# Kernel optimization log

Hardware: AMD Instinct MI355X
Metric: run time of the kernel (lower is better)

## Reference

```python
import jax, jax.numpy as jnp
import numpy as np

EPS = 1e-7
MIN_NORM = 1e-15
PROJ_EPS = 1e-5
NEG_SLOPE = 0.2
HEADS = 4


def artanh(x):
    return jnp.arctanh(jnp.clip(x, -1.0 + EPS, 1.0 - EPS))


def _norm(x):
    return jnp.clip(jnp.linalg.norm(x, axis=-1, keepdims=True), MIN_NORM)


def proj(x):
    # project onto Poincare ball (c=1)
    n = _norm(x)
    maxn = 1.0 - PROJ_EPS
    return jnp.where(n > maxn, x / n * maxn, x)


def expmap0(u):
    n = _norm(u)
    return jnp.tanh(n) * u / n


def logmap0(x):
    n = _norm(x)
    return artanh(n) * x / n


def mobius_add(x, y):
    x2 = jnp.sum(x * x, axis=-1, keepdims=True)
    y2 = jnp.sum(y * y, axis=-1, keepdims=True)
    xy = jnp.sum(x * y, axis=-1, keepdims=True)
    num = (1.0 + 2.0 * xy + y2) * x + (1.0 - x2) * y
    den = 1.0 + 2.0 * xy + x2 * y2
    return num / jnp.clip(den, MIN_NORM)


def pdist(x, y):
    # Poincare distance, c=1 -> [...,] scalar
    ma = mobius_add(-x, y)
    return 2.0 * artanh(jnp.linalg.norm(ma, axis=-1))


def mobius_scalar_mul(r, x):
    n = _norm(x)
    return jnp.tanh(r * artanh(n)) * x / n


def mobius_matvec(W, x):
    # x: [N,din], W: [dout,din]
    mx = x @ W.T
    n_x = _norm(x)
    n_mx = _norm(mx)
    return jnp.tanh(n_mx / n_x * artanh(n_x)) * mx / n_mx


def segment_softmax(logits, seg, num_segments):
    m = jax.ops.segment_max(logits, seg, num_segments=num_segments)
    m = jnp.where(jnp.isfinite(m), m, 0.0)
    e = jnp.exp(logits - m[seg])
    s = jax.ops.segment_sum(e, seg, num_segments=num_segments)
    return e / (s[seg] + 1e-16)


def setup_inputs() -> dict:
    N, E, D = 50000, 500000, 128
    H = HEADS
    Dh = D // H
    ks = jax.random.split(jax.random.key(0), 12)
    # edges without self-loops (reference re-adds them, mirroring remove/add_self_loops)
    src = jax.random.randint(ks[0], (E,), 0, N)
    off = jax.random.randint(ks[1], (E,), 1, N)
    dst = (src + off) % N
    edge_index = jnp.stack([src, dst]).astype(jnp.int32)
    x_e = 0.1 * jax.random.normal(ks[2], (N, D), dtype=jnp.float32)
    x_h = proj(expmap0(0.05 * jax.random.normal(ks[3], (N, D), dtype=jnp.float32)))
    sc = 1.0 / np.sqrt(D)
    W_e = sc * jax.random.normal(ks[4], (D, D), dtype=jnp.float32)
    b_lin_e = jnp.zeros((D,), jnp.float32)
    att_e = 0.1 * jax.random.normal(ks[5], (1, H, 2 * Dh), dtype=jnp.float32)
    b_e = jnp.zeros((D,), jnp.float32)
    W_h = sc * jax.random.normal(ks[6], (D, D), dtype=jnp.float32)
    b_lin_h = jnp.zeros((D,), jnp.float32)
    att_h = 0.1 * jax.random.normal(ks[7], (1, H, 2 * Dh), dtype=jnp.float32)
    b_h = jnp.zeros((D,), jnp.float32)
    att_hf = 0.1 * jax.random.normal(ks[8], (1, 1), dtype=jnp.float32)
    att_ef = 0.1 * jax.random.normal(ks[9], (1, 1), dtype=jnp.float32)
    return {"x_e": x_e, "x_h": x_h, "edge_index": edge_index,
            "W_e": W_e, "b_lin_e": b_lin_e, "att_e": att_e, "b_e": b_e,
            "W_h": W_h, "b_lin_h": b_lin_h, "att_h": att_h, "b_h": b_h,
            "att_hf": att_hf, "att_ef": att_ef}


def reference(x_e, x_h, edge_index, W_e, b_lin_e, att_e, b_e,
              W_h, b_lin_h, att_h, b_h, att_hf, att_ef):
    N, D = x_e.shape
    H = HEADS
    Dh = att_e.shape[-1] // 2
    loop = jnp.arange(N, dtype=edge_index.dtype)
    src = jnp.concatenate([edge_index[0], loop])  # j (source)
    dst = jnp.concatenate([edge_index[1], loop])  # i (target, softmax segment)

    # ---- Euclidean GAT branch (GATConv) ----
    xe = (x_e @ W_e.T + b_lin_e).reshape(N, H, Dh)
    a_i = jnp.sum(xe * att_e[:, :, :Dh], axis=-1)  # [N,H] target part
    a_j = jnp.sum(xe * att_e[:, :, Dh:], axis=-1)  # [N,H] source part
    alpha = jax.nn.leaky_relu(a_i[dst] + a_j[src], NEG_SLOPE)  # [E',H]
    alpha = segment_softmax(alpha, dst, N)
    agg = jax.ops.segment_sum(xe[src] * alpha[:, :, None], dst, num_segments=N)
    e_out = jax.nn.relu(agg.reshape(N, H * Dh) + b_e)

    # ---- Hyperbolic GAT branch (HGATConv with HypLinear) ----
    mv = proj(mobius_matvec(W_h, x_h))
    hb = proj(expmap0(b_lin_h))  # proj_tan0 is identity on Poincare ball
    xh = proj(mobius_add(mv, hb))  # [N,D] hyperbolic points (original_x)
    lx = logmap0(xh).reshape(N, H, Dh)
    hi = jnp.sum(lx * att_h[:, :, :Dh], axis=-1)
    hj = jnp.sum(lx * att_h[:, :, Dh:], axis=-1)
    alpha_h = hi[dst] + hj[src]  # [E',H]
    d = pdist(xh[dst], xh[src])  # [E'] hyperbolic edge distances
    d = segment_softmax(d, dst, N)[:, None]
    alpha_h = jax.nn.leaky_relu(alpha_h * d, NEG_SLOPE)
    alpha_h = segment_softmax(alpha_h, dst, N)
    agg_h = jax.ops.segment_sum(lx[src] * alpha_h[:, :, None], dst, num_segments=N)
    out_t = jax.nn.relu(agg_h.reshape(N, H * Dh) + b_h)  # tangent at origin
    h_out = proj(expmap0(out_t))

    # ---- HFusion: fuse Euclidean into hyperbolic ----
    ye = proj(expmap0(e_out))
    dist_f = (pdist(h_out, ye) * att_hf[0, 0])[:, None]  # [N,1]
    xe2 = proj(mobius_scalar_mul(dist_f, ye))
    h_fused = proj(mobius_add(h_out, xe2))

    # ---- EFusion: fuse hyperbolic into Euclidean ----
    lh = logmap0(h_out)
    de = (jnp.sum((lh - e_out) ** 2, axis=-1) * att_ef[0, 0])[:, None]
    e_fused = e_out + de * lh

    return jnp.stack([h_fused, e_fused])  # [2,N,D]
```

## Files before the change

### kernel.cpp

```cpp
#include <hip/hip_runtime.h>
#include <hip/hip_fp16.h>
#include <math.h>

typedef _Float16 h2 __attribute__((ext_vector_type(2)));
typedef _Float16 h8 __attribute__((ext_vector_type(8)));
typedef float f32x4 __attribute__((ext_vector_type(4)));

#define MAXN_BALL (1.0f - 1e-5f)
#define ART_CLIP  (1.0f - 1e-7f)
#define MAXD 48

__device__ __forceinline__ float f_rcp(float x)  { return __builtin_amdgcn_rcpf(x); }
__device__ __forceinline__ float f_exp(float x)  { return __expf(x); }
__device__ __forceinline__ float f_log(float x)  { return __logf(x); }
__device__ __forceinline__ float f_tanh(float x) {
    float ax = fabsf(x);
    float e = __expf(2.f * ax);
    float t = 1.f - 2.f * f_rcp(e + 1.f);
    return copysignf(t, x);
}
__device__ __forceinline__ float f_atanh(float x) {
    x = fminf(x, ART_CLIP);
    return 0.5f * f_log((1.f + x) * f_rcp(1.f - x));
}
__device__ __forceinline__ float leaky(float x) { return x > 0.0f ? x : 0.2f * x; }

union F4H8 { float4 f; h2 h[4]; };
union F2H4 { float2 f; h2 h[2]; };
union H8U  { h8 v; h2 h[4]; };
union H8F  { float4 f; h8 v; h2 h[4]; };

__device__ __forceinline__ h2 pk16(float x, float y) {
    union { decltype(__builtin_amdgcn_cvt_pkrtz(0.f, 0.f)) a; h2 b; } u;
    u.a = __builtin_amdgcn_cvt_pkrtz(x, y);
    return u.b;
}

__global__ __launch_bounds__(256) void k_wcvt(const float* __restrict__ W0,
                                              const float* __restrict__ W1,
                                              h2* __restrict__ W16,
                                              int* __restrict__ counts,
                                              int N, int cblocks) {
    int b = blockIdx.x, t = threadIdx.x;
    if (b < cblocks) {
        int zi = b * 256 + t;
        if (zi < N) counts[zi] = 0;
        return;
    }
    int tw = (b - cblocks) * 256 + t;
    const float* W = (tw < 2048) ? W0 : W1;
    int c = (tw & 2047) * 8;
    float4 a = *(const float4*)(W + c);
    float4 bb = *(const float4*)(W + c + 4);
    F4H8 u;
    u.h[0] = pk16(a.x, a.y);  u.h[1] = pk16(a.z, a.w);
    u.h[2] = pk16(bb.x, bb.y); u.h[3] = pk16(bb.z, bb.w);
    *(float4*)&W16[(tw >> 11) * 8192 + (c >> 1)] = u.f;
}

__global__ __launch_bounds__(256) void k_prep(const float* __restrict__ X0,
                                              const float* __restrict__ X1,
                                              const h2* __restrict__ W16,
                                              const float* __restrict__ bias0,
                                              const float* __restrict__ att_e,
                                              h2* __restrict__ Y0,
                                              h2* __restrict__ Y1,
                                              float* __restrict__ aux_j,
                                              float* __restrict__ aux_i,
                                              float* __restrict__ aux_n,
                                              const int* __restrict__ ei,
                                              int* __restrict__ counts,
                                              int* __restrict__ srcs,
                                              int N, int E) {
    int t = threadIdx.x;
    if (blockIdx.y == 2) {
        int idx = blockIdx.x * 256 + t;
        if (idx < E + N) {
            int s, d;
            if (idx < E) { s = ei[idx]; d = ei[E + idx]; } else { s = d = idx - E; }
            int p = atomicAdd(&counts[d], 1);
            if (p < MAXD) srcs[d * MAXD + p] = s;
        }
        return;
    }
    int wv = t >> 6, l = t & 63;
    int rt = blockIdx.x * 4 + wv;
    if (rt * 32 >= N) return;
    int mat = blockIdx.y;
    const float* X = mat ? X1 : X0;
    const h2* Wbase = W16 + mat * 8192;
    h2* Y = mat ? Y1 : Y0;

    int lane16 = l & 15, quad = l >> 4;
    int r0 = rt * 32 + lane16, r1 = r0 + 16;
    int rr0 = (r0 < N) ? r0 : (N - 1);
    int rr1 = (r1 < N) ? r1 : (N - 1);
    const float* Xrow0 = &X[(size_t)rr0 * 128 + quad * 8];
    const float* Xrow1 = &X[(size_t)rr1 * 128 + quad * 8];

    H8U b0r[4], b1r[4];
    float nx20 = 0.f, nx21 = 0.f;
#pragma unroll
    for (int ks = 0; ks < 4; ++ks) {
        float4 xa = *(const float4*)(Xrow0 + ks * 32);
        float4 xb = *(const float4*)(Xrow0 + ks * 32 + 4);
        if (mat) nx20 += xa.x * xa.x + xa.y * xa.y + xa.z * xa.z + xa.w * xa.w
                       + xb.x * xb.x + xb.y * xb.y + xb.z * xb.z + xb.w * xb.w;
        b0r[ks].h[0] = pk16(xa.x, xa.y); b0r[ks].h[1] = pk16(xa.z, xa.w);
        b0r[ks].h[2] = pk16(xb.x, xb.y); b0r[ks].h[3] = pk16(xb.z, xb.w);
        float4 ya = *(const float4*)(Xrow1 + ks * 32);
        float4 yb = *(const float4*)(Xrow1 + ks * 32 + 4);
        if (mat) nx21 += ya.x * ya.x + ya.y * ya.y + ya.z * ya.z + ya.w * ya.w
                       + yb.x * yb.x + yb.y * yb.y + yb.z * yb.z + yb.w * yb.w;
        b1r[ks].h[0] = pk16(ya.x, ya.y); b1r[ks].h[1] = pk16(ya.z, ya.w);
        b1r[ks].h[2] = pk16(yb.x, yb.y); b1r[ks].h[3] = pk16(yb.z, yb.w);
    }

    float pi0[4] = {0.f, 0.f, 0.f, 0.f}, pj0[4] = {0.f, 0.f, 0.f, 0.f};
    float pi1[4] = {0.f, 0.f, 0.f, 0.f}, pj1[4] = {0.f, 0.f, 0.f, 0.f};
#pragma unroll
    for (int ct = 0; ct < 8; ++ct) {
        const h2* Wrow = &Wbase[(ct * 16 + lane16) * 64 + quad * 4];
        f32x4 acc0 = {0.f, 0.f, 0.f, 0.f};
        f32x4 acc1 = {0.f, 0.f, 0.f, 0.f};
#pragma unroll
        for (int ks = 0; ks < 4; ++ks) {
            H8F a;
            a.f = *(const float4*)(Wrow + ks * 16);
            acc0 = __builtin_amdgcn_mfma_f32_16x16x32_f16(a.v, b0r[ks].v, acc0, 0, 0, 0);
            acc1 = __builtin_amdgcn_mfma_f32_16x16x32_f16(a.v, b1r[ks].v, acc1, 0, 0, 0);
        }
        int obase = ct * 16 + quad * 4;
        if (mat == 0) {
            float4 bb = *(const float4*)&bias0[obase];
            F2H4 u0, u1;
            u0.h[0] = pk16(acc0[0] + bb.x, acc0[1] + bb.y);
            u0.h[1] = pk16(acc0[2] + bb.z, acc0[3] + bb.w);
            u1.h[0] = pk16(acc1[0] + bb.x, acc1[1] + bb.y);
            u1.h[1] = pk16(acc1[2] + bb.z, acc1[3] + bb.w);
            if (r0 < N) *(float2*)&Y[(size_t)r0 * 64 + (obase >> 1)] = u0.f;
            if (r1 < N) *(float2*)&Y[(size_t)r1 * 64 + (obase >> 1)] = u1.f;
            float4 xe40 = make_float4((float)u0.h[0].x, (float)u0.h[0].y,
                                      (float)u0.h[1].x, (float)u0.h[1].y);
            float4 xe41 = make_float4((float)u1.h[0].x, (float)u1.h[0].y,
                                      (float)u1.h[1].x, (float)u1.h[1].y);
            int hd = ct >> 1, w0 = (ct & 1) * 16 + quad * 4;
            float4 aT = *(const float4*)&att_e[hd * 64 + w0];
            float4 aS = *(const float4*)&att_e[hd * 64 + 32 + w0];
            pi0[hd] += xe40.x * aT.x + xe40.y * aT.y + xe40.z * aT.z + xe40.w * aT.w;
            pj0[hd] += xe40.x * aS.x + xe40.y * aS.y + xe40.z * aS.z + xe40.w * aS.w;
            pi1[hd] += xe41.x * aT.x + xe41.y * aT.y + xe41.z * aT.z + xe41.w * aT.w;
            pj1[hd] += xe41.x * aS.x + xe41.y * aS.y + xe41.z * aS.z + xe41.w * aS.w;
        } else {
            F2H4 u0, u1;
            u0.h[0] = pk16(acc0[0], acc0[1]); u0.h[1] = pk16(acc0[2], acc0[3]);
            u1.h[0] = pk16(acc1[0], acc1[1]); u1.h[1] = pk16(acc1[2], acc1[3]);
            if (r0 < N) *(float2*)&Y[(size_t)r0 * 64 + (obase >> 1)] = u0.f;
            if (r1 < N) *(float2*)&Y[(size_t)r1 * 64 + (obase >> 1)] = u1.f;
        }
    }

    if (mat == 0) {
#pragma unroll
        for (int m = 16; m <= 32; m <<= 1) {
#pragma unroll
            for (int hd = 0; hd < 4; ++hd) {
                pi0[hd] += __shfl_xor(pi0[hd], m, 64);
                pj0[hd] += __shfl_xor(pj0[hd], m, 64);
                pi1[hd] += __shfl_xor(pi1[hd], m, 64);
                pj1[hd] += __shfl_xor(pj1[hd], m, 64);
            }
        }
        if (quad == 0) {
            if (r0 < N) {
                *(float4*)&aux_i[(size_t)r0 * 8 + 4]  = make_float4(pi0[0], pi0[1], pi0[2], pi0[3]);
                *(float4*)&aux_j[(size_t)r0 * 16 + 4] = make_float4(pj0[0], pj0[1], pj0[2], pj0[3]);
            }
            if (r1 < N) {
                *(float4*)&aux_i[(size_t)r1 * 8 + 4]  = make_float4(pi1[0], pi1[1], pi1[2], pi1[3]);
                *(float4*)&aux_j[(size_t)r1 * 16 + 4] = make_float4(pj1[0], pj1[1], pj1[2], pj1[3]);
            }
        }
    } else {
#pragma unroll
        for (int m = 16; m <= 32; m <<= 1) {
            nx20 += __shfl_xor(nx20, m, 64);
            nx21 += __shfl_xor(nx21, m, 64);
        }
        if (quad == 0) {
            if (r0 < N) aux_n[r0] = nx20;
            if (r1 < N) aux_n[r1] = nx21;
        }
    }
}

__global__ __launch_bounds__(256) void k_node1(
        const float* __restrict__ aux_n, const h2* __restrict__ mx16,
        h2* __restrict__ xh16,
        float* __restrict__ aux_j, float* __restrict__ aux_i,
        const float* __restrict__ att_h, const float* __restrict__ b_lin_h,
        int N) {
    int t = threadIdx.x;
    int sl = t & 31, ni = t >> 5;
    int i = blockIdx.x * 8 + ni;
    if (i >= N) return;
    int ht = sl >> 3, d0 = (sl & 7) * 4;

    F2H4 umx; umx.f = *(const float2*)&mx16[(size_t)i * 64 + 2 * sl];
    float4 mx4 = make_float4((float)umx.h[0].x, (float)umx.h[0].y,
                             (float)umx.h[1].x, (float)umx.h[1].y);
    float4 bv4 = *(const float4*)&b_lin_h[4 * sl];
    float nmx2 = mx4.x * mx4.x + mx4.y * mx4.y + mx4.z * mx4.z + mx4.w * mx4.w;
    float nb2  = bv4.x * bv4.x + bv4.y * bv4.y + bv4.z * bv4.z + bv4.w * bv4.w;
    float dmb  = mx4.x * bv4.x + mx4.y * bv4.y + mx4.z * bv4.z + mx4.w * bv4.w;
#pragma unroll
    for (int m = 16; m >= 1; m >>= 1) {
        nmx2 += __shfl_xor(nmx2, m, 64);
        nb2  += __shfl_xor(nb2, m, 64);
        dmb  += __shfl_xor(dmb, m, 64);
    }
    float nx2 = aux_n[i];

    float nxr = sqrtf(nx2),  nxc = fmaxf(nxr, 1e-15f);
    float nmxr = sqrtf(nmx2), nmxc = fmaxf(nmxr, 1e-15f);
    float tt = f_tanh(nmxc * f_rcp(nxc) * f_atanh(nxc));
    float c_m = tt * f_rcp(nmxc);
    float nmv = tt * (nmxr * f_rcp(nmxc));
    if (nmv > MAXN_BALL) { c_m *= MAXN_BALL / nmv; nmv = MAXN_BALL; }

    float nbr = sqrtf(nb2), nbc = fmaxf(nbr, 1e-15f);
    float tb = f_tanh(nbc);
    float c_b = tb * f_rcp(nbc);
    float nhb = tb * (nbr * f_rcp(nbc));
    if (nhb > MAXN_BALL) { c_b *= MAXN_BALL / nhb; nhb = MAXN_BALL; }

    float xy = c_m * c_b * dmb;
    float x2 = nmv * nmv, y2 = nhb * nhb;
    float den = fmaxf(1.f + 2.f * xy + x2 * y2, 1e-15f);
    float rden = f_rcp(den);
    float al = (1.f + 2.f * xy + y2) * c_m * rden;
    float be = (1.f - x2) * c_b * rden;
    float nr2 = al * al * nmx2 + 2.f * al * be * dmb + be * be * nb2;
    float nrr = sqrtf(nr2);
    if (nrr > MAXN_BALL) { float sc = MAXN_BALL / nrr; al *= sc; be *= sc; }
    float4 resv;
    resv.x = al * mx4.x + be * bv4.x; resv.y = al * mx4.y + be * bv4.y;
    resv.z = al * mx4.z + be * bv4.z; resv.w = al * mx4.w + be * bv4.w;
    F2H4 st;
    st.h[0] = pk16(resv.x, resv.y);
    st.h[1] = pk16(resv.z, resv.w);
    *(float2*)&xh16[(size_t)i * 64 + 2 * sl] = st.f;
    float4 rv = make_float4((float)st.h[0].x, (float)st.h[0].y,
                            (float)st.h[1].x, (float)st.h[1].y);

    float nr2r = rv.x * rv.x + rv.y * rv.y + rv.z * rv.z + rv.w * rv.w;
#pragma unroll
    for (int m = 16; m >= 1; m >>= 1) nr2r += __shfl_xor(nr2r, m, 64);
    float nrrr = sqrtf(nr2r);
    float nnc = fmaxf(nrrr, 1e-15f);
    float lam = f_atanh(nnc) * f_rcp(nnc);
    if (sl == 0) { aux_j[(size_t)i * 16 + 8] = lam; aux_j[(size_t)i * 16 + 9] = nr2r; }

    float4 lxv = make_float4(lam * rv.x, lam * rv.y, lam * rv.z, lam * rv.w);
    float4 ahT = *(const float4*)&att_h[ht * 64 + d0];
    float4 ahS = *(const float4*)&att_h[ht * 64 + 32 + d0];
    float qi = lxv.x * ahT.x + lxv.y * ahT.y + lxv.z * ahT.z + lxv.w * ahT.w;
    float qj = lxv.x * ahS.x + lxv.y * ahS.y + lxv.z * ahS.z + lxv.w * ahS.w;
#pragma unroll
    for (int m = 1; m <= 4; m <<= 1) { qi += __shfl_xor(qi, m, 64); qj += __shfl_xor(qj, m, 64); }
    if ((sl & 7) == 0) {
        aux_j[(size_t)i * 16 + ht] = qj;
        aux_i[(size_t)i * 8 + ht] = qi;
    }
}

__global__ __launch_bounds__(256) void k_node_final(
    const h2* __restrict__ xh16, const float* __restrict__ aux_j,
    const float* __restrict__ aux_i, const h2* __restrict__ xe16,
    const int* __restrict__ counts, const int* __restrict__ srcs,
    const float* __restrict__ b_e, const float* __restrict__ b_h,
    const float* __restrict__ att_hf, const float* __restrict__ att_ef,
    float* __restrict__ out, int N) {
    __shared__ int   s_src_all[8][MAXD];
    __shared__ float s_d_all[8][MAXD];
    __shared__ float s_ah_all[8][MAXD * 4];
    __shared__ float s_ae_all[8][MAXD * 4];

    int t = threadIdx.x;
    int sl = t & 31, ni = t >> 5;
    int i = blockIdx.x * 8 + ni;
    if (i >= N) return;
    int*   s_src = s_src_all[ni];
    float* s_d   = s_d_all[ni];
    float* s_ah  = s_ah_all[ni];
    float* s_ae  = s_ae_all[ni];

    int deg = counts[i];
    if (deg > MAXD) deg = MAXD;
    if (sl < deg)      s_src[sl]      = srcs[i * MAXD + sl];
    if (sl + 32 < deg) s_src[sl + 32] = srcs[i * MAXD + sl + 32];

    float x2i = aux_j[(uint32_t)i * 16u + 9u];
    {
        int g = sl & 7, sub = sl >> 3;
        uint32_t goff = (uint32_t)(g * 8);
        const h2* xi = &xh16[(uint32_t)i * 64u + goff];
        F4H8 us0, us1;
        us0.f = *(const float4*)xi;
        us1.f = *(const float4*)(xi + 4);
        for (int p = 0; p * 4 < deg; ++p) {
            int e = p * 4 + sub;
            bool act = e < deg;
            float dot = 0.f;
            int j = 0;
            if (act) {
                j = s_src[e];
                uint32_t oj = (uint32_t)j * 64u + goff;
                F4H8 ua, ub;
                ua.f = *(const float4*)&xh16[oj];
                ub.f = *(const float4*)&xh16[oj + 4u];
#pragma unroll
                for (int k = 0; k < 4; ++k) dot = __builtin_amdgcn_fdot2(ua.h[k], us0.h[k], dot, false);
#pragma unroll
                for (int k = 0; k < 4; ++k) dot = __builtin_amdgcn_fdot2(ub.h[k], us1.h[k], dot, false);
            }
            dot += __shfl_xor(dot, 1, 64);
            dot += __shfl_xor(dot, 2, 64);
            dot += __shfl_xor(dot, 4, 64);
            if (act && g == 0) {
                float y2 = aux_j[(uint32_t)j * 16u + 9u];
                float xy = dot;
                float A = 1.f - 2.f * xy + y2;
                float B = 1.f - x2i;
                float den = fmaxf(1.f - 2.f * xy + x2i * y2, 1e-15f);
                float num2 = fmaxf(A * A * x2i - 2.f * A * B * xy + B * B * y2, 0.f);
                float nma = fminf(sqrtf(num2) * f_rcp(den), ART_CLIP);
                s_d[e] = f_log((1.f + nma) * f_rcp(1.f - nma));
            }
        }
    }

    float eA = (sl < deg)      ? f_exp(s_d[sl])      : 0.f;
    float eB = (sl + 32 < deg) ? f_exp(s_d[sl + 32]) : 0.f;
    float ssum = eA + eB;
#pragma unroll
    for (int m = 16; m >= 1; m >>= 1) ssum += __shfl_xor(ssum, m, 64);
    float dinv = f_rcp(ssum + 1e-16f);

    float4 hi4 = *(const float4*)&aux_i[(uint32_t)i * 8u];
    float4 ai4 = *(const float4*)&aux_i[(uint32_t)i * 8u + 4u];
    float4 vh_s[2], ve_s[2];
    float lam_s[2] = {0.f, 0.f};
    float4 sh = make_float4(0.f, 0.f, 0.f, 0.f), se = sh;
#pragma unroll
    for (int s = 0; s < 2; ++s) {
        int e = sl + 32 * s;
        if (e < deg) {
            int j = s_src[e];
            float ds = (s ? eB : eA) * dinv;
            uint32_t oj = (uint32_t)j * 16u;
            float4 hj4 = *(const float4*)&aux_j[oj];
            float4 aj4 = *(const float4*)&aux_j[oj + 4u];
            lam_s[s] = aux_j[oj + 8u];
            float4 vh, ve;
            vh.x = f_exp(leaky((hi4.x + hj4.x) * ds));
            vh.y = f_exp(leaky((hi4.y + hj4.y) * ds));
            vh.z = f_exp(leaky((hi4.z + hj4.z) * ds));
            vh.w = f_exp(leaky((hi4.w + hj4.w) * ds));
            ve.x = f_exp(leaky(ai4.x + aj4.x));
            ve.y = f_exp(leaky(ai4.y + aj4.y));
            ve.z = f_exp(leaky(ai4.z + aj4.z));
            ve.w = f_exp(leaky(ai4.w + aj4.w));
            vh_s[s] = vh; ve_s[s] = ve;
            sh.x += vh.x; sh.y += vh.y; sh.z += vh.z; sh.w += vh.w;
            se.x += ve.x; se.y += ve.y; se.z += ve.z; se.w += ve.w;
        }
    }
#pragma unroll
    for (int m = 16; m >= 1; m >>= 1) {
        sh.x += __shfl_xor(sh.x, m, 64); sh.y += __shfl_xor(sh.y, m, 64);
        sh.z += __shfl_xor(sh.z, m, 64); sh.w += __shfl_xor(sh.w, m, 64);
        se.x += __shfl_xor(se.x, m, 64); se.y += __shfl_xor(se.y, m, 64);
        se.z += __shfl_xor(se.z, m, 64); se.w += __shfl_xor(se.w, m, 64);
    }
    float4 rh = make_float4(f_rcp(sh.x + 1e-16f), f_rcp(sh.y + 1e-16f),
                            f_rcp(sh.z + 1e-16f), f_rcp(sh.w + 1e-16f));
    float4 re = make_float4(f_rcp(se.x + 1e-16f), f_rcp(se.y + 1e-16f),
                            f_rcp(se.z + 1e-16f), f_rcp(se.w + 1e-16f));
#pragma unroll
    for (int s = 0; s < 2; ++s) {
        int e = sl + 32 * s;
        if (e < deg) {
            float lamj = lam_s[s];
            float4 vh = vh_s[s], ve = ve_s[s];
            vh.x *= rh.x * lamj; vh.y *= rh.y * lamj; vh.z *= rh.z * lamj; vh.w *= rh.w * lamj;
            ve.x *= re.x; ve.y *= re.y; ve.z *= re.z; ve.w *= re.w;
            *(float4*)&s_ah[e * 4] = vh;
            *(float4*)&s_ae[e * 4] = ve;
        }
    }

    int hq = sl >> 3;
    uint32_t dsl = 2u * (uint32_t)sl;
    float4 aE = make_float4(0.f, 0.f, 0.f, 0.f), aH = aE;
    int e = 0;
    for (; e + 3 < deg; e += 4) {
        int j0 = s_src[e], j1 = s_src[e + 1], j2 = s_src[e + 2], j3 = s_src[e + 3];
        uint32_t o0 = (uint32_t)j0 * 64u + dsl, o1 = (uint32_t)j1 * 64u + dsl;
        uint32_t o2 = (uint32_t)j2 * 64u + dsl, o3 = (uint32_t)j3 * 64u + dsl;
        F2H4 ux0, uh0, ux1, uh1, ux2, uh2, ux3, uh3;
        ux0.f = *(const float2*)&xe16[o0]; uh0.f = *(const float2*)&xh16[o0];
        ux1.f = *(const float2*)&xe16[o1]; uh1.f = *(const float2*)&xh16[o1];
        ux2.f = *(const float2*)&xe16[o2]; uh2.f = *(const float2*)&xh16[o2];
        ux3.f = *(const float2*)&xe16[o3]; uh3.f = *(const float2*)&xh16[o3];
        float we0 = s_ae[e * 4 + hq],       wh0 = s_ah[e * 4 + hq];
        float we1 = s_ae[(e + 1) * 4 + hq], wh1 = s_ah[(e + 1) * 4 + hq];
        float we2 = s_ae[(e + 2) * 4 + hq], wh2 = s_ah[(e + 2) * 4 + hq];
        float we3 = s_ae[(e + 3) * 4 + hq], wh3 = s_ah[(e + 3) * 4 + hq];
        aE.x += we0 * (float)ux0.h[0].x + we1 * (float)ux1.h[0].x;
        aE.y += we0 * (float)ux0.h[0].y + we1 * (float)ux1.h[0].y;
        aE.z += we0 * (float)ux0.h[1].x + we1 * (float)ux1.h[1].x;
        aE.w += we0 * (float)ux0.h[1].y + we1 * (float)ux1.h[1].y;
        aH.x += wh0 * (float)uh0.h[0].x + wh1 * (float)uh1.h[0].x;
        aH.y += wh0 * (float)uh0.h[0].y + wh1 * (float)uh1.h[0].y;
        aH.z += wh0 * (float)uh0.h[1].x + wh1 * (float)uh1.h[1].x;
        aH.w += wh0 * (float)uh0.h[1].y + wh1 * (float)uh1.h[1].y;
        aE.x += we2 * (float)ux2.h[0].x + we3 * (float)ux3.h[0].x;
        aE.y += we2 * (float)ux2.h[0].y + we3 * (float)ux3.h[0].y;
        aE.z += we2 * (float)ux2.h[1].x + we3 * (float)ux3.h[1].x;
        aE.w += we2 * (float)ux2.h[1].y + we3 * (float)ux3.h[1].y;
        aH.x += wh2 * (float)uh2.h[0].x + wh3 * (float)uh3.h[0].x;
        aH.y += wh2 * (float)uh2.h[0].y + wh3 * (float)uh3.h[0].y;
        aH.z += wh2 * (float)uh2.h[1].x + wh3 * (float)uh3.h[1].x;
        aH.w += wh2 * (float)uh2.h[1].y + wh3 * (float)uh3.h[1].y;
    }
    for (; e + 1 < deg; e += 2) {
        int j0 = s_src[e], j1 = s_src[e + 1];
        uint32_t o0 = (uint32_t)j0 * 64u + dsl, o1 = (uint32_t)j1 * 64u + dsl;
        F2H4 ux0, uh0, ux1, uh1;
        ux0.f = *(const float2*)&xe16[o0]; uh0.f = *(const float2*)&xh16[o0];
        ux1.f = *(const float2*)&xe16[o1]; uh1.f = *(const float2*)&xh16[o1];
        float we0 = s_ae[e * 4 + hq], wh0 = s_ah[e * 4 + hq];
        float we1 = s_ae[(e + 1) * 4 + hq], wh1 = s_ah[(e + 1) * 4 + hq];
        aE.x += we0 * (float)ux0.h[0].x + we1 * (float)ux1.h[0].x;
        aE.y += we0 * (float)ux0.h[0].y + we1 * (float)ux1.h[0].y;
        aE.z += we0 * (float)ux0.h[1].x + we1 * (float)ux1.h[1].x;
        aE.w += we0 * (float)ux0.h[1].y + we1 * (float)ux1.h[1].y;
        aH.x += wh0 * (float)uh0.h[0].x + wh1 * (float)uh1.h[0].x;
        aH.y += wh0 * (float)uh0.h[0].y + wh1 * (float)uh1.h[0].y;
        aH.z += wh0 * (float)uh0.h[1].x + wh1 * (float)uh1.h[1].x;
        aH.w += wh0 * (float)uh0.h[1].y + wh1 * (float)uh1.h[1].y;
    }
    if (e < deg) {
        int j = s_src[e];
        uint32_t oj = (uint32_t)j * 64u + dsl;
        F2H4 ux, uh;
        ux.f = *(const float2*)&xe16[oj];
        uh.f = *(const float2*)&xh16[oj];
        float we = s_ae[e * 4 + hq], wh = s_ah[e * 4 + hq];
        aE.x += we * (float)ux.h[0].x; aE.y += we * (float)ux.h[0].y;
        aE.z += we * (float)ux.h[1].x; aE.w += we * (float)ux.h[1].y;
        aH.x += wh * (float)uh.h[0].x; aH.y += wh * (float)uh.h[0].y;
        aH.z += wh * (float)uh.h[1].x; aH.w += wh * (float)uh.h[1].y;
    }

    float4 be4 = *(const float4*)&b_e[4 * sl];
    float4 bh4 = *(const float4*)&b_h[4 * sl];
    float4 eo, ot;
    eo.x = fmaxf(aE.x + be4.x, 0.f); eo.y = fmaxf(aE.y + be4.y, 0.f);
    eo.z = fmaxf(aE.z + be4.z, 0.f); eo.w = fmaxf(aE.w + be4.w, 0.f);
    ot.x = fmaxf(aH.x + bh4.x, 0.f); ot.y = fmaxf(aH.y + bh4.y, 0.f);
    ot.z = fmaxf(aH.z + bh4.z, 0.f); ot.w = fmaxf(aH.w + bh4.w, 0.f);
    float n2  = ot.x * ot.x + ot.y * ot.y + ot.z * ot.z + ot.w * ot.w;
    float ne2 = eo.x * eo.x + eo.y * eo.y + eo.z * eo.z + eo.w * eo.w;
    float dot3 = ot.x * eo.x + ot.y * eo.y + ot.z * eo.z + ot.w * eo.w;
#pragma unroll
    for (int m = 16; m >= 1; m >>= 1) {
        n2 += __shfl_xor(n2, m, 64); ne2 += __shfl_xor(ne2, m, 64); dot3 += __shfl_xor(dot3, m, 64);
    }

    float n_raw = sqrtf(n2), n_c = fmaxf(n_raw, 1e-15f);
    float th = f_tanh(n_c);
    float c_h = th * f_rcp(n_c);
    float nh = th * (n_raw * f_rcp(n_c));
    if (nh > MAXN_BALL) { c_h *= MAXN_BALL / nh; nh = MAXN_BALL; }

    float nE_raw = sqrtf(ne2), nE_c = fmaxf(nE_raw, 1e-15f);
    float tE = f_tanh(nE_c);
    float c_e = tE * f_rcp(nE_c);
    float ny = tE * (nE_raw * f_rcp(nE_c));
    if (ny > MAXN_BALL) { c_e *= MAXN_BALL / ny; ny = MAXN_BALL; }

    float xyv = c_h * c_e * dot3;
    float x2f = nh * nh, y2f = ny * ny;
    float A = 1.f - 2.f * xyv + y2f, B = 1.f - x2f;
    float den = fmaxf(1.f - 2.f * xyv + x2f * y2f, 1e-15f);
    float num2 = fmaxf(A * A * x2f - 2.f * A * B * xyv + B * B * y2f, 0.f);
    float nma = fminf(sqrtf(num2) * f_rcp(den), ART_CLIP);
    float distf = f_log((1.f + nma) * f_rcp(1.f - nma)) * att_hf[0];
    float nyc = fmaxf(ny, 1e-15f);
    float s1 = f_tanh(distf * f_atanh(nyc)) * f_rcp(nyc);
    float nxe2 = fabsf(s1) * ny;
    if (nxe2 > MAXN_BALL) { s1 *= MAXN_BALL / nxe2; nxe2 = MAXN_BALL; }
    float xy2 = s1 * xyv;
    float y22 = nxe2 * nxe2;
    float rden2 = f_rcp(fmaxf(1.f + 2.f * xy2 + x2f * y22, 1e-15f));
    float alpha = (1.f + 2.f * xy2 + y22) * rden2 * c_h;
    float beta  = (1.f - x2f) * s1 * rden2 * c_e;
    float nf2 = alpha * alpha * n2 + 2.f * alpha * beta * dot3 + beta * beta * ne2;
    float nf = sqrtf(nf2);
    if (nf > MAXN_BALL) { float sc = MAXN_BALL / nf; alpha *= sc; beta *= sc; }

    float nhc = fmaxf(nh, 1e-15f);
    float gam = f_atanh(nhc) * f_rcp(nhc) * c_h;
    float de2 = gam * gam * n2 - 2.f * gam * dot3 + ne2;
    float dg = de2 * att_ef[0] * gam;

    float4 o1;
    o1.x = alpha * ot.x + beta * eo.x; o1.y = alpha * ot.y + beta * eo.y;
    o1.z = alpha * ot.z + beta * eo.z; o1.w = alpha * ot.w + beta * eo.w;
    *(float4*)&out[(size_t)i * 128 + 4 * sl] = o1;
    float4 o2;
    o2.x = eo.x + dg * ot.x; o2.y = eo.y + dg * ot.y;
    o2.z = eo.z + dg * ot.z; o2.w = eo.w + dg * ot.w;
    *(float4*)&out[(size_t)N * 128 + (size_t)i * 128 + 4 * sl] = o2;
}

extern "C" void kernel_launch(void* const* d_in, const int* in_sizes, int n_in,
                              void* d_out, int out_size, void* d_ws, size_t ws_size,
                              hipStream_t stream) {
    const float* x_e      = (const float*)d_in[0];
    const float* x_h      = (const float*)d_in[1];
    const int*   ei       = (const int*)d_in[2];
    const float* W_e      = (const float*)d_in[3];
    const float* b_lin_e  = (const float*)d_in[4];
    const float* att_e    = (const float*)d_in[5];
    const float* b_e      = (const float*)d_in[6];
    const float* W_h      = (const float*)d_in[7];
    const float* b_lin_h  = (const float*)d_in[8];
    const float* att_h    = (const float*)d_in[9];
    const float* b_h      = (const float*)d_in[10];
    const float* att_hf   = (const float*)d_in[11];
    const float* att_ef   = (const float*)d_in[12];

    int N = in_sizes[0] / 128;
    int E = in_sizes[2] / 2;
    int EN = E + N;

    char* ws = (char*)d_ws;
    size_t off = 0;
    auto alloc = [&](size_t bytes) -> void* {
        void* p = ws + off;
        off = (off + bytes + 255) & ~(size_t)255;
        return p;
    };
    h2*    W16   = (h2*)alloc((size_t)2 * 8192 * 4);
    h2*    xe16  = (h2*)alloc((size_t)N * 128 * 2);
    h2*    mx16  = (h2*)alloc((size_t)N * 128 * 2);
    h2*    xh16  = (h2*)alloc((size_t)N * 128 * 2);
    float* aux_j = (float*)alloc((size_t)N * 16 * 4);
    float* aux_i = (float*)alloc((size_t)N * 8 * 4);
    float* aux_n = (float*)alloc((size_t)N * 4);
    int*   counts= (int*)alloc((size_t)N * 4);
    int*   srcs  = (int*)alloc((size_t)N * MAXD * 4);

    int cblocks = (N + 255) / 256;
    k_wcvt<<<cblocks + 16, 256, 0, stream>>>(W_e, W_h, W16, counts, N, cblocks);

    int rtiles = (N + 31) / 32;
    int rblocks = (rtiles + 3) / 4;
    int eblocks = (EN + 255) / 256;
    int gx = rblocks > eblocks ? rblocks : eblocks;
    dim3 pgrid(gx, 3);
    k_prep<<<pgrid, 256, 0, stream>>>(x_e, x_h, W16, b_lin_e, att_e,
                                      xe16, mx16, aux_j, aux_i, aux_n,
                                      ei, counts, srcs, N, E);

    int nblocks = (N + 7) / 8;
    k_node1<<<nblocks, 256, 0, stream>>>(aux_n, mx16, xh16, aux_j, aux_i,
                                         att_h, b_lin_h, N);

    int fblocks = (N + 7) / 8;
    k_node_final<<<fblocks, 256, 0, stream>>>(xh16, aux_j, aux_i, xe16,
                                              counts, srcs, b_e, b_h, att_hf, att_ef,
                                              (float*)d_out, N);
}
```

Baseline: 242.8 us.

## Interleave Euclidean and hyperbolic node features for single-load neighbor gathers

Stores the fp16 Euclidean projection and the hyperbolic tangent features interleaved per node in one buffer, four halfs of each per slice, so the aggregation loop fetches both with one 16-byte load per neighbor instead of two 8-byte loads. To fit this layout, the prep GEMM drops from two 16-row tiles per wave to one, and node1 writes its hyperbolic output a second time into the interleaved buffer. The intent is fewer gather transactions in the edge-bound final kernel, paid for by the extra store, fewer rows of work per wave in prep, and a larger buffer.

```diff
diff --git a/kernel.cpp b/kernel.cpp
--- a/kernel.cpp
+++ b/kernel.cpp
@@ -63,8 +63,8 @@
                                               const h2* __restrict__ W16,
                                               const float* __restrict__ bias0,
                                               const float* __restrict__ att_e,
-                                              h2* __restrict__ Y0,
-                                              h2* __restrict__ Y1,
+                                              h2* __restrict__ xeh,
+                                              h2* __restrict__ mx16,
                                               float* __restrict__ aux_j,
                                               float* __restrict__ aux_i,
                                               float* __restrict__ aux_n,
@@ -85,78 +85,57 @@
     }
     int wv = t >> 6, l = t & 63;
     int rt = blockIdx.x * 4 + wv;
-    if (rt * 32 >= N) return;
+    if (rt * 16 >= N) return;
     int mat = blockIdx.y;
     const float* X = mat ? X1 : X0;
     const h2* Wbase = W16 + mat * 8192;
-    h2* Y = mat ? Y1 : Y0;
 
     int lane16 = l & 15, quad = l >> 4;
-    int r0 = rt * 32 + lane16, r1 = r0 + 16;
-    int rr0 = (r0 < N) ? r0 : (N - 1);
-    int rr1 = (r1 < N) ? r1 : (N - 1);
-    const float* Xrow0 = &X[(size_t)rr0 * 128 + quad * 8];
-    const float* Xrow1 = &X[(size_t)rr1 * 128 + quad * 8];
-
-    H8U b0r[4], b1r[4];
-    float nx20 = 0.f, nx21 = 0.f;
+    int r = rt * 16 + lane16;
+    int rr = (r < N) ? r : (N - 1);
+    const float* Xrow = &X[(size_t)rr * 128 + quad * 8];
+
+    H8U bfr[4];
+    float nx2 = 0.f;
 #pragma unroll
     for (int ks = 0; ks < 4; ++ks) {
-        float4 xa = *(const float4*)(Xrow0 + ks * 32);
-        float4 xb = *(const float4*)(Xrow0 + ks * 32 + 4);
-        if (mat) nx20 += xa.x * xa.x + xa.y * xa.y + xa.z * xa.z + xa.w * xa.w
-                       + xb.x * xb.x + xb.y * xb.y + xb.z * xb.z + xb.w * xb.w;
-        b0r[ks].h[0] = pk16(xa.x, xa.y); b0r[ks].h[1] = pk16(xa.z, xa.w);
-        b0r[ks].h[2] = pk16(xb.x, xb.y); b0r[ks].h[3] = pk16(xb.z, xb.w);
-        float4 ya = *(const float4*)(Xrow1 + ks * 32);
-        float4 yb = *(const float4*)(Xrow1 + ks * 32 + 4);
-        if (mat) nx21 += ya.x * ya.x + ya.y * ya.y + ya.z * ya.z + ya.w * ya.w
-                       + yb.x * yb.x + yb.y * yb.y + yb.z * yb.z + yb.w * yb.w;
-        b1r[ks].h[0] = pk16(ya.x, ya.y); b1r[ks].h[1] = pk16(ya.z, ya.w);
-        b1r[ks].h[2] = pk16(yb.x, yb.y); b1r[ks].h[3] = pk16(yb.z, yb.w);
-    }
-
-    float pi0[4] = {0.f, 0.f, 0.f, 0.f}, pj0[4] = {0.f, 0.f, 0.f, 0.f};
-    float pi1[4] = {0.f, 0.f, 0.f, 0.f}, pj1[4] = {0.f, 0.f, 0.f, 0.f};
+        float4 xa = *(const float4*)(Xrow + ks * 32);
+        float4 xb = *(const float4*)(Xrow + ks * 32 + 4);
+        if (mat) nx2 += xa.x * xa.x + xa.y * xa.y + xa.z * xa.z + xa.w * xa.w
+                      + xb.x * xb.x + xb.y * xb.y + xb.z * xb.z + xb.w * xb.w;
+        bfr[ks].h[0] = pk16(xa.x, xa.y); bfr[ks].h[1] = pk16(xa.z, xa.w);
+        bfr[ks].h[2] = pk16(xb.x, xb.y); bfr[ks].h[3] = pk16(xb.z, xb.w);
+    }
+
+    float pi[4] = {0.f, 0.f, 0.f, 0.f}, pj[4] = {0.f, 0.f, 0.f, 0.f};
 #pragma unroll
     for (int ct = 0; ct < 8; ++ct) {
         const h2* Wrow = &Wbase[(ct * 16 + lane16) * 64 + quad * 4];
-        f32x4 acc0 = {0.f, 0.f, 0.f, 0.f};
-        f32x4 acc1 = {0.f, 0.f, 0.f, 0.f};
+        f32x4 acc = {0.f, 0.f, 0.f, 0.f};
 #pragma unroll
         for (int ks = 0; ks < 4; ++ks) {
             H8F a;
             a.f = *(const float4*)(Wrow + ks * 16);
-            acc0 = __builtin_amdgcn_mfma_f32_16x16x32_f16(a.v, b0r[ks].v, acc0, 0, 0, 0);
-            acc1 = __builtin_amdgcn_mfma_f32_16x16x32_f16(a.v, b1r[ks].v, acc1, 0, 0, 0);
+            acc = __builtin_amdgcn_mfma_f32_16x16x32_f16(a.v, bfr[ks].v, acc, 0, 0, 0);
         }
         int obase = ct * 16 + quad * 4;
         if (mat == 0) {
             float4 bb = *(const float4*)&bias0[obase];
-            F2H4 u0, u1;
-            u0.h[0] = pk16(acc0[0] + bb.x, acc0[1] + bb.y);
-            u0.h[1] = pk16(acc0[2] + bb.z, acc0[3] + bb.w);
-            u1.h[0] = pk16(acc1[0] + bb.x, acc1[1] + bb.y);
-            u1.h[1] = pk16(acc1[2] + bb.z, acc1[3] + bb.w);
-            if (r0 < N) *(float2*)&Y[(size_t)r0 * 64 + (obase >> 1)] = u0.f;
-            if (r1 < N) *(float2*)&Y[(size_t)r1 * 64 + (obase >> 1)] = u1.f;
-            float4 xe40 = make_float4((float)u0.h[0].x, (float)u0.h[0].y,
-                                      (float)u0.h[1].x, (float)u0.h[1].y);
-            float4 xe41 = make_float4((float)u1.h[0].x, (float)u1.h[0].y,
-                                      (float)u1.h[1].x, (float)u1.h[1].y);
+            F2H4 u;
+            u.h[0] = pk16(acc[0] + bb.x, acc[1] + bb.y);
+            u.h[1] = pk16(acc[2] + bb.z, acc[3] + bb.w);
+            if (r < N) *(float2*)&xeh[(size_t)r * 128 + 16 * ct + 4 * quad] = u.f;
+            float4 xe4 = make_float4((float)u.h[0].x, (float)u.h[0].y,
+                                     (float)u.h[1].x, (float)u.h[1].y);
             int hd = ct >> 1, w0 = (ct & 1) * 16 + quad * 4;
             float4 aT = *(const float4*)&att_e[hd * 64 + w0];
             float4 aS = *(const float4*)&att_e[hd * 64 + 32 + w0];
-            pi0[hd] += xe40.x * aT.x + xe40.y * aT.y + xe40.z * aT.z + xe40.w * aT.w;
-            pj0[hd] += xe40.x * aS.x + xe40.y * aS.y + xe40.z * aS.z + xe40.w * aS.w;
-            pi1[hd] += xe41.x * aT.x + xe41.y * aT.y + xe41.z * aT.z + xe41.w * aT.w;
-            pj1[hd] += xe41.x * aS.x + xe41.y * aS.y + xe41.z * aS.z + xe41.w * aS.w;
+            pi[hd] += xe4.x * aT.x + xe4.y * aT.y + xe4.z * aT.z + xe4.w * aT.w;
+            pj[hd] += xe4.x * aS.x + xe4.y * aS.y + xe4.z * aS.z + xe4.w * aS.w;
         } else {
-            F2H4 u0, u1;
-            u0.h[0] = pk16(acc0[0], acc0[1]); u0.h[1] = pk16(acc0[2], acc0[3]);
-            u1.h[0] = pk16(acc1[0], acc1[1]); u1.h[1] = pk16(acc1[2], acc1[3]);
-            if (r0 < N) *(float2*)&Y[(size_t)r0 * 64 + (obase >> 1)] = u0.f;
-            if (r1 < N) *(float2*)&Y[(size_t)r1 * 64 + (obase >> 1)] = u1.f;
+            F2H4 u;
+            u.h[0] = pk16(acc[0], acc[1]); u.h[1] = pk16(acc[2], acc[3]);
+            if (r < N) *(float2*)&mx16[(size_t)r * 64 + (obase >> 1)] = u.f;
         }
     }
 
@@ -165,38 +144,24 @@
         for (int m = 16; m <= 32; m <<= 1) {
 #pragma unroll
             for (int hd = 0; hd < 4; ++hd) {
-                pi0[hd] += __shfl_xor(pi0[hd], m, 64);
-                pj0[hd] += __shfl_xor(pj0[hd], m, 64);
-                pi1[hd] += __shfl_xor(pi1[hd], m, 64);
-                pj1[hd] += __shfl_xor(pj1[hd], m, 64);
+                pi[hd] += __shfl_xor(pi[hd], m, 64);
+                pj[hd] += __shfl_xor(pj[hd], m, 64);
             }
         }
-        if (quad == 0) {
-            if (r0 < N) {
-                *(float4*)&aux_i[(size_t)r0 * 8 + 4]  = make_float4(pi0[0], pi0[1], pi0[2], pi0[3]);
-                *(float4*)&aux_j[(size_t)r0 * 16 + 4] = make_float4(pj0[0], pj0[1], pj0[2], pj0[3]);
-            }
-            if (r1 < N) {
-                *(float4*)&aux_i[(size_t)r1 * 8 + 4]  = make_float4(pi1[0], pi1[1], pi1[2], pi1[3]);
-                *(float4*)&aux_j[(size_t)r1 * 16 + 4] = make_float4(pj1[0], pj1[1], pj1[2], pj1[3]);
-            }
+        if (quad == 0 && r < N) {
+            *(float4*)&aux_i[(size_t)r * 8 + 4]  = make_float4(pi[0], pi[1], pi[2], pi[3]);
+            *(float4*)&aux_j[(size_t)r * 16 + 4] = make_float4(pj[0], pj[1], pj[2], pj[3]);
         }
     } else {
 #pragma unroll
-        for (int m = 16; m <= 32; m <<= 1) {
-            nx20 += __shfl_xor(nx20, m, 64);
-            nx21 += __shfl_xor(nx21, m, 64);
-        }
-        if (quad == 0) {
-            if (r0 < N) aux_n[r0] = nx20;
-            if (r1 < N) aux_n[r1] = nx21;
-        }
+        for (int m = 16; m <= 32; m <<= 1) nx2 += __shfl_xor(nx2, m, 64);
+        if (quad == 0 && r < N) aux_n[r] = nx2;
     }
 }
 
 __global__ __launch_bounds__(256) void k_node1(
         const float* __restrict__ aux_n, const h2* __restrict__ mx16,
-        h2* __restrict__ xh16,
+        h2* __restrict__ xh16, h2* __restrict__ xeh,
         float* __restrict__ aux_j, float* __restrict__ aux_i,
         const float* __restrict__ att_h, const float* __restrict__ b_lin_h,
         int N) {
@@ -250,6 +215,7 @@
     st.h[0] = pk16(resv.x, resv.y);
     st.h[1] = pk16(resv.z, resv.w);
     *(float2*)&xh16[(size_t)i * 64 + 2 * sl] = st.f;
+    *(float2*)&xeh[(size_t)i * 128 + 4 * sl + 2] = st.f;
     float4 rv = make_float4((float)st.h[0].x, (float)st.h[0].y,
                             (float)st.h[1].x, (float)st.h[1].y);
 
@@ -276,7 +242,7 @@
 
 __global__ __launch_bounds__(256) void k_node_final(
     const h2* __restrict__ xh16, const float* __restrict__ aux_j,
-    const float* __restrict__ aux_i, const h2* __restrict__ xe16,
+    const float* __restrict__ aux_i, const h2* __restrict__ xeh,
     const int* __restrict__ counts, const int* __restrict__ srcs,
     const float* __restrict__ b_e, const float* __restrict__ b_h,
     const float* __restrict__ att_hf, const float* __restrict__ att_ef,
@@ -401,67 +367,62 @@
     }
 
     int hq = sl >> 3;
-    uint32_t dsl = 2u * (uint32_t)sl;
+    uint32_t dsl = 4u * (uint32_t)sl;
     float4 aE = make_float4(0.f, 0.f, 0.f, 0.f), aH = aE;
     int e = 0;
     for (; e + 3 < deg; e += 4) {
         int j0 = s_src[e], j1 = s_src[e + 1], j2 = s_src[e + 2], j3 = s_src[e + 3];
-        uint32_t o0 = (uint32_t)j0 * 64u + dsl, o1 = (uint32_t)j1 * 64u + dsl;
-        uint32_t o2 = (uint32_t)j2 * 64u + dsl, o3 = (uint32_t)j3 * 64u + dsl;
-        F2H4 ux0, uh0, ux1, uh1, ux2, uh2, ux3, uh3;
-        ux0.f = *(const float2*)&xe16[o0]; uh0.f = *(const float2*)&xh16[o0];
-        ux1.f = *(const float2*)&xe16[o1]; uh1.f = *(const float2*)&xh16[o1];
-        ux2.f = *(const float2*)&xe16[o2]; uh2.f = *(const float2*)&xh16[o2];
-        ux3.f = *(const float2*)&xe16[o3]; uh3.f = *(const float2*)&xh16[o3];
+        F4H8 u0, u1, u2, u3;
+        u0.f = *(const float4*)&xeh[(uint32_t)j0 * 128u + dsl];
+        u1.f = *(const float4*)&xeh[(uint32_t)j1 * 128u + dsl];
+        u2.f = *(const float4*)&xeh[(uint32_t)j2 * 128u + dsl];
+        u3.f = *(const float4*)&xeh[(uint32_t)j3 * 128u + dsl];
         float we0 = s_ae[e * 4 + hq],       wh0 = s_ah[e * 4 + hq];
         float we1 = s_ae[(e + 1) * 4 + hq], wh1 = s_ah[(e + 1) * 4 + hq];
         float we2 = s_ae[(e + 2) * 4 + hq], wh2 = s_ah[(e + 2) * 4 + hq];
         float we3 = s_ae[(e + 3) * 4 + hq], wh3 = s_ah[(e + 3) * 4 + hq];
-        aE.x += we0 * (float)ux0.h[0].x + we1 * (float)ux1.h[0].x;
-        aE.y += we0 * (float)ux0.h[0].y + we1 * (float)ux1.h[0].y;
-        aE.z += we0 * (float)ux0.h[1].x + we1 * (float)ux1.h[1].x;
-        aE.w += we0 * (float)ux0.h[1].y + we1 * (float)ux1.h[1].y;
-        aH.x += wh0 * (float)uh0.h[0].x + wh1 * (float)uh1.h[0].x;
-        aH.y += wh0 * (float)uh0.h[0].y + wh1 * (float)uh1.h[0].y;
-        aH.z += wh0 * (float)uh0.h[1].x + wh1 * (float)uh1.h[1].x;
-        aH.w += wh0 * (float)uh0.h[1].y + wh1 * (float)uh1.h[1].y;
-        aE.x += we2 * (float)ux2.h[0].x + we3 * (float)ux3.h[0].x;
-        aE.y += we2 * (float)ux2.h[0].y + we3 * (float)ux3.h[0].y;
-        aE.z += we2 * (float)ux2.h[1].x + we3 * (float)ux3.h[1].x;
-        aE.w += we2 * (float)ux2.h[1].y + we3 * (float)ux3.h[1].y;
-        aH.x += wh2 * (float)uh2.h[0].x + wh3 * (float)uh3.h[0].x;
-        aH.y += wh2 * (float)uh2.h[0].y + wh3 * (float)uh3.h[0].y;
-        aH.z += wh2 * (float)uh2.h[1].x + wh3 * (float)uh3.h[1].x;
-        aH.w += wh2 * (float)uh2.h[1].y + wh3 * (float)uh3.h[1].y;
+        aE.x += we0 * (float)u0.h[0].x + we1 * (float)u1.h[0].x;
+        aE.y += we0 * (float)u0.h[0].y + we1 * (float)u1.h[0].y;
+        aE.z += we0 * (float)u0.h[1].x + we1 * (float)u1.h[1].x;
+        aE.w += we0 * (float)u0.h[1].y + we1 * (float)u1.h[1].y;
+        aH.x += wh0 * (float)u0.h[2].x + wh1 * (float)u1.h[2].x;
+        aH.y += wh0 * (float)u0.h[2].y + wh1 * (float)u1.h[2].y;
+        aH.z += wh0 * (float)u0.h[3].x + wh1 * (float)u1.h[3].x;
+        aH.w += wh0 * (float)u0.h[3].y + wh1 * (float)u1.h[3].y;
+        aE.x += we2 * (float)u2.h[0].x + we3 * (float)u3.h[0].x;
+        aE.y += we2 * (float)u2.h[0].y + we3 * (float)u3.h[0].y;
+        aE.z += we2 * (float)u2.h[1].x + we3 * (float)u3.h[1].x;
+        aE.w += we2 * (float)u2.h[1].y + we3 * (float)u3.h[1].y;
+        aH.x += wh2 * (float)u2.h[2].x + wh3 * (float)u3.h[2].x;
+        aH.y += wh2 * (float)u2.h[2].y + wh3 * (float)u3.h[2].y;
+        aH.z += wh2 * (float)u2.h[3].x + wh3 * (float)u3.h[3].x;
+        aH.w += wh2 * (float)u2.h[3].y + wh3 * (float)u3.h[3].y;
     }
     for (; e + 1 < deg; e += 2) {
         int j0 = s_src[e], j1 = s_src[e + 1];
-        uint32_t o0 = (uint32_t)j0 * 64u + dsl, o1 = (uint32_t)j1 * 64u + dsl;
-        F2H4 ux0, uh0, ux1, uh1;
-        ux0.f = *(const float2*)&xe16[o0]; uh0.f = *(const float2*)&xh16[o0];
-        ux1.f = *(const float2*)&xe16[o1]; uh1.f = *(const float2*)&xh16[o1];
+        F4H8 u0, u1;
+        u0.f = *(const float4*)&xeh[(uint32_t)j0 * 128u + dsl];
+        u1.f = *(const float4*)&xeh[(uint32_t)j1 * 128u + dsl];
         float we0 = s_ae[e * 4 + hq], wh0 = s_ah[e * 4 + hq];
         float we1 = s_ae[(e + 1) * 4 + hq], wh1 = s_ah[(e + 1) * 4 + hq];
-        aE.x += we0 * (float)ux0.h[0].x + we1 * (float)ux1.h[0].x;
-        aE.y += we0 * (float)ux0.h[0].y + we1 * (float)ux1.h[0].y;
-        aE.z += we0 * (float)ux0.h[1].x + we1 * (float)ux1.h[1].x;
-        aE.w += we0 * (float)ux0.h[1].y + we1 * (float)ux1.h[1].y;
-        aH.x += wh0 * (float)uh0.h[0].x + wh1 * (float)uh1.h[0].x;
-        aH.y += wh0 * (float)uh0.h[0].y + wh1 * (float)uh1.h[0].y;
-        aH.z += wh0 * (float)uh0.h[1].x + wh1 * (float)uh1.h[1].x;
-        aH.w += wh0 * (float)uh0.h[1].y + wh1 * (float)uh1.h[1].y;
+        aE.x += we0 * (float)u0.h[0].x + we1 * (float)u1.h[0].x;
+        aE.y += we0 * (float)u0.h[0].y + we1 * (float)u1.h[0].y;
+        aE.z += we0 * (float)u0.h[1].x + we1 * (float)u1.h[1].x;
+        aE.w += we0 * (float)u0.h[1].y + we1 * (float)u1.h[1].y;
+        aH.x += wh0 * (float)u0.h[2].x + wh1 * (float)u1.h[2].x;
+        aH.y += wh0 * (float)u0.h[2].y + wh1 * (float)u1.h[2].y;
+        aH.z += wh0 * (float)u0.h[3].x + wh1 * (float)u1.h[3].x;
+        aH.w += wh0 * (float)u0.h[3].y + wh1 * (float)u1.h[3].y;
     }
     if (e < deg) {
         int j = s_src[e];
-        uint32_t oj = (uint32_t)j * 64u + dsl;
-        F2H4 ux, uh;
-        ux.f = *(const float2*)&xe16[oj];
-        uh.f = *(const float2*)&xh16[oj];
+        F4H8 u0;
+        u0.f = *(const float4*)&xeh[(uint32_t)j * 128u + dsl];
         float we = s_ae[e * 4 + hq], wh = s_ah[e * 4 + hq];
-        aE.x += we * (float)ux.h[0].x; aE.y += we * (float)ux.h[0].y;
-        aE.z += we * (float)ux.h[1].x; aE.w += we * (float)ux.h[1].y;
-        aH.x += wh * (float)uh.h[0].x; aH.y += wh * (float)uh.h[0].y;
-        aH.z += wh * (float)uh.h[1].x; aH.w += wh * (float)uh.h[1].y;
+        aE.x += we * (float)u0.h[0].x; aE.y += we * (float)u0.h[0].y;
+        aE.z += we * (float)u0.h[1].x; aE.w += we * (float)u0.h[1].y;
+        aH.x += wh * (float)u0.h[2].x; aH.y += wh * (float)u0.h[2].y;
+        aH.z += wh * (float)u0.h[3].x; aH.w += wh * (float)u0.h[3].y;
     }
 
     float4 be4 = *(const float4*)&b_e[4 * sl];
@@ -555,7 +516,7 @@
         return p;
     };
     h2*    W16   = (h2*)alloc((size_t)2 * 8192 * 4);
-    h2*    xe16  = (h2*)alloc((size_t)N * 128 * 2);
+    h2*    xeh   = (h2*)alloc((size_t)N * 128 * 4);
     h2*    mx16  = (h2*)alloc((size_t)N * 128 * 2);
     h2*    xh16  = (h2*)alloc((size_t)N * 128 * 2);
     float* aux_j = (float*)alloc((size_t)N * 16 * 4);
@@ -567,21 +528,21 @@
     int cblocks = (N + 255) / 256;
     k_wcvt<<<cblocks + 16, 256, 0, stream>>>(W_e, W_h, W16, counts, N, cblocks);
 
-    int rtiles = (N + 31) / 32;
+    int rtiles = (N + 15) / 16;
     int rblocks = (rtiles + 3) / 4;
     int eblocks = (EN + 255) / 256;
     int gx = rblocks > eblocks ? rblocks : eblocks;
     dim3 pgrid(gx, 3);
     k_prep<<<pgrid, 256, 0, stream>>>(x_e, x_h, W16, b_lin_e, att_e,
-                                      xe16, mx16, aux_j, aux_i, aux_n,
+                                      xeh, mx16, aux_j, aux_i, aux_n,
                                       ei, counts, srcs, N, E);
 
     int nblocks = (N + 7) / 8;
-    k_node1<<<nblocks, 256, 0, stream>>>(aux_n, mx16, xh16, aux_j, aux_i,
+    k_node1<<<nblocks, 256, 0, stream>>>(aux_n, mx16, xh16, xeh, aux_j, aux_i,
                                          att_h, b_lin_h, N);
 
     int fblocks = (N + 7) / 8;
-    k_node_final<<<fblocks, 256, 0, stream>>>(xh16, aux_j, aux_i, xe16,
+    k_node_final<<<fblocks, 256, 0, stream>>>(xh16, aux_j, aux_i, xeh,
                                               counts, srcs, b_e, b_h, att_hf, att_ef,
                                               (float*)d_out, N);
 }
```

After: 253.6 us. +4.5%, slower.
